# Performance work log

Measured on AMD Instinct MI355X. Metric: run time of the kernel, lower is better.

The kernel has to match this reference:

```python
import jax, jax.numpy as jnp
import numpy as np

N = 50000   # nodes
E = 800000  # edges (avg degree 16)
D = 128     # dim (in == out per layer)
R = 8       # num_relations
B = 4       # num_bases
L = 2       # conv_layer_num
EPS = 1e-5      # LayerNorm eps
SLOPE = 0.2     # leaky_relu negative slope


def setup_inputs() -> dict:
    key = jax.random.key(0)
    ks = jax.random.split(key, 10)
    s = 0.05
    x = jax.random.normal(ks[0], (N, D), dtype=jnp.float32)
    edge_index = jax.random.randint(ks[1], (2, E), 0, N)
    edge_type = jax.random.randint(ks[2], (E,), 0, R)
    basis = jax.random.normal(ks[3], (L, B, D, D), dtype=jnp.float32) * s
    att_r = jax.random.normal(ks[4], (L, R, B), dtype=jnp.float32) * s
    att = jax.random.normal(ks[5], (L, 2 * D), dtype=jnp.float32) * s
    root = jax.random.normal(ks[6], (L, D, D), dtype=jnp.float32) * s
    bias = jax.random.normal(ks[7], (L, D), dtype=jnp.float32) * s
    ln_w = jnp.ones((L, D), dtype=jnp.float32)
    ln_b = jnp.zeros((L, D), dtype=jnp.float32)
    return {"x": x, "edge_index": edge_index, "edge_type": edge_type,
            "basis": basis, "att_r": att_r, "att": att, "root": root,
            "bias": bias, "ln_w": ln_w, "ln_b": ln_b}


def _gnn_layer(x, src, dst, et, basis, att_r, att, root, bias, ln_w, ln_b):
    # relation weights from bases: [R, D, D]
    w = jnp.einsum('rb,bio->rio', att_r, basis)
    # transform all nodes under all relations once, then gather per edge
    xw = jnp.einsum('ni,rio->rno', x, w)          # [R, N, D]
    x_j = xw[et, src]                              # [E, D] relation-specific src msg
    xr = x @ root                                  # [N, D] root transform
    x_i = xr[dst]                                  # [E, D]
    # attention: (cat[x_i, x_j] * att).sum(-1), leaky_relu, segment softmax by dst
    alpha = x_i @ att[:D] + x_j @ att[D:]          # [E]
    alpha = jnp.where(alpha > 0, alpha, SLOPE * alpha)
    amax = jax.ops.segment_max(alpha, dst, num_segments=N)
    amax = jnp.where(jnp.isfinite(amax), amax, 0.0)
    ex = jnp.exp(alpha - amax[dst])
    denom = jax.ops.segment_sum(ex, dst, num_segments=N)
    alpha = ex / (denom[dst] + 1e-16)
    # weighted scatter-add aggregation (dropout rate = 0 -> identity)
    aggr = jax.ops.segment_sum(x_j * alpha[:, None], dst, num_segments=N)  # [N, D]
    out = aggr + xr + bias
    # LayerNorm
    mu = out.mean(-1, keepdims=True)
    var = out.var(-1, keepdims=True)
    out = (out - mu) / jnp.sqrt(var + EPS) * ln_w + ln_b
    return jnp.tanh(out)


def reference(x, edge_index, edge_type, basis, att_r, att, root, bias, ln_w, ln_b):
    src, dst = edge_index[0], edge_index[1]
    states = []
    for l in range(L):
        x = _gnn_layer(x, src, dst, edge_type, basis[l], att_r[l], att[l],
                       root[l], bias[l], ln_w[l], ln_b[l])
        states.append(x)
    return (x, jnp.stack(states))
```

## Files before the change

kernel.cpp:

```cpp
#include <hip/hip_runtime.h>
#include <math.h>

#define D 128
#define NB 4
#define NR 8
#define NLAYER 2
#define KTOT 640
#define EPSV 1e-5f
#define SLOPE 0.2f
#define NBUK 32
#define BSHIFT 11

typedef __attribute__((ext_vector_type(8))) short short8;
typedef __attribute__((ext_vector_type(4))) float f32x4;

__device__ __forceinline__ unsigned short f2bf(float f) {
  unsigned u = __float_as_uint(f);
  u += 0x7FFF + ((u >> 16) & 1);
  return (unsigned short)(u >> 16);
}

__device__ __forceinline__ float block_sum_128(float v, volatile float* scratch) {
#pragma unroll
  for (int off = 32; off > 0; off >>= 1) v += __shfl_xor(v, off);
  __syncthreads();
  if ((threadIdx.x & 63) == 0) scratch[threadIdx.x >> 6] = v;
  __syncthreads();
  return scratch[0] + scratch[1];
}

__global__ void hist_kernel(const int* __restrict__ dst, int* __restrict__ deg, int E) {
  int e = blockIdx.x * 256 + threadIdx.x;
  if (e < E) atomicAdd(&deg[dst[e]], 1);
}

__global__ void __launch_bounds__(1024) scan_kernel(const int* __restrict__ deg,
                                                    int* __restrict__ offs,
                                                    int* __restrict__ cur,
                                                    int* __restrict__ bcur, int n) {
  __shared__ int wsums[16];
  const int tid = threadIdx.x, lane = tid & 63, wid = tid >> 6;
  int carry = 0;
  for (int base = 0; base < n; base += 4096) {
    int i0 = base + tid * 4;
    int v0 = 0, v1 = 0, v2 = 0, v3 = 0;
    if (i0 + 3 < n) {
      int4 q = *(const int4*)(deg + i0);
      v0 = q.x; v1 = q.y; v2 = q.z; v3 = q.w;
    } else if (i0 < n) {
      v0 = deg[i0];
      if (i0 + 1 < n) v1 = deg[i0 + 1];
      if (i0 + 2 < n) v2 = deg[i0 + 2];
    }
    int tsum = v0 + v1 + v2 + v3;
    int x = tsum;
#pragma unroll
    for (int off = 1; off < 64; off <<= 1) {
      int y = __shfl_up(x, off);
      if (lane >= off) x += y;
    }
    if (lane == 63) wsums[wid] = x;
    __syncthreads();
    if (wid == 0) {
      int ws = (lane < 16) ? wsums[lane] : 0;
#pragma unroll
      for (int off = 1; off < 16; off <<= 1) {
        int y = __shfl_up(ws, off);
        if (lane >= off) ws += y;
      }
      if (lane < 16) wsums[lane] = ws;
    }
    __syncthreads();
    int prefix = carry + ((wid > 0) ? wsums[wid - 1] : 0) + x - tsum;
    int e0 = prefix, e1 = e0 + v0, e2 = e1 + v1, e3 = e2 + v2;
    if (i0 < n)     { offs[i0] = e0;     cur[i0] = e0; }
    if (i0 + 1 < n) { offs[i0 + 1] = e1; cur[i0 + 1] = e1; }
    if (i0 + 2 < n) { offs[i0 + 2] = e2; cur[i0 + 2] = e2; }
    if (i0 + 3 < n) { offs[i0 + 3] = e3; cur[i0 + 3] = e3; }
    int btot = wsums[15];
    __syncthreads();
    carry += btot;
  }
  if (tid == 0) offs[n] = carry;
  __syncthreads();
  if (tid < NBUK) {
    int idx = tid << BSHIFT;
    bcur[tid * 16] = offs[idx < n ? idx : n];
  }
}

__global__ void __launch_bounds__(1024) bucket_kernel(
    const int* __restrict__ src, const int* __restrict__ dst, const int* __restrict__ et,
    int* __restrict__ bcur, unsigned long long* __restrict__ ebuf, int E) {
  __shared__ int lcnt[NBUK];
  __shared__ int lbase[NBUK];
  const int tid = threadIdx.x;
  const int e = blockIdx.x * 1024 + tid;
  if (tid < NBUK) lcnt[tid] = 0;
  __syncthreads();
  int d = 0, b = 0, rank = 0;
  unsigned pk = 0;
  bool valid = e < E;
  if (valid) {
    d = dst[e];
    pk = (unsigned)src[e] | ((unsigned)et[e] << 16);
    b = d >> BSHIFT;
    rank = atomicAdd(&lcnt[b], 1);
  }
  __syncthreads();
  if (tid < NBUK && lcnt[tid] > 0) lbase[tid] = atomicAdd(&bcur[tid * 16], lcnt[tid]);
  __syncthreads();
  if (valid) ebuf[lbase[b] + rank] = ((unsigned long long)(unsigned)d << 32) | pk;
}

__global__ void scatter2_kernel(const unsigned long long* __restrict__ ebuf,
                                int* __restrict__ cur, unsigned* __restrict__ csr, int E) {
  int e = blockIdx.x * 256 + threadIdx.x;
  if (e < E) {
    unsigned long long r = ebuf[e];
    int d = (int)(r >> 32);
    int pos = atomicAdd(&cur[d], 1);
    csr[pos] = (unsigned)r;
  }
}

__global__ void __launch_bounds__(128) prep_w(const float* __restrict__ basis,
                                              const float* __restrict__ root,
                                              const float* __restrict__ att,
                                              unsigned short* __restrict__ BT0,
                                              unsigned short* __restrict__ BT1,
                                              float* __restrict__ av0, float* __restrict__ av1) {
  __shared__ float scratch[2];
  int k = blockIdx.x, l = 0;
  if (k >= KTOT) { k -= KTOT; l = 1; }
  const float* basis_l = basis + (size_t)l * NB * D * D;
  const float* root_l  = root + (size_t)l * D * D;
  const float* att_l   = att + (size_t)l * 2 * D;
  unsigned short* BT = l ? BT1 : BT0;
  float* av = l ? av1 : av0;
  const int o = threadIdx.x;
  float v = (k < 512) ? basis_l[(size_t)(k >> 7) * (D * D) + (size_t)(k & 127) * D + o]
                      : root_l[(size_t)(k - 512) * D + o];
  BT[(size_t)o * KTOT + k] = f2bf(v);
  float w = (k < 512) ? att_l[D + o] : att_l[o];
  float s = block_sum_128(v * w, scratch);
  if (o == 0) av[k] = s;
}

__global__ void __launch_bounds__(256) prep_xa(const float* __restrict__ x0,
                                               const float* __restrict__ av,
                                               unsigned short* __restrict__ ga,
                                               float* __restrict__ ai,
                                               float* __restrict__ ajb, int N, int Npad) {
  int n = blockIdx.x * 4 + (threadIdx.x >> 6);
  int lane = threadIdx.x & 63;
  if (n >= Npad) return;
  if (n >= N) {
    *(unsigned*)(ga + (size_t)n * KTOT + 512 + 2 * lane) = 0;
    return;
  }
  float2 xv = *(const float2*)(x0 + (size_t)n * D + 2 * lane);
  unsigned packed = (unsigned)f2bf(xv.x) | ((unsigned)f2bf(xv.y) << 16);
  *(unsigned*)(ga + (size_t)n * KTOT + 512 + 2 * lane) = packed;
  float d[5];
#pragma unroll
  for (int b = 0; b < 4; ++b) {
    float2 w = *(const float2*)(av + b * D + 2 * lane);
    d[b] = xv.x * w.x + xv.y * w.y;
  }
  {
    float2 w = *(const float2*)(av + 512 + 2 * lane);
    d[4] = xv.x * w.x + xv.y * w.y;
  }
#pragma unroll
  for (int off = 1; off < 64; off <<= 1) {
#pragma unroll
    for (int i = 0; i < 5; ++i) d[i] += __shfl_xor(d[i], off);
  }
  if (lane == 0) {
    *(float4*)(ajb + (size_t)n * 4) = make_float4(d[0], d[1], d[2], d[3]);
    ai[n] = d[4];
  }
}

__global__ void __launch_bounds__(256) a2_kernel(const unsigned short* __restrict__ ga,
                                                 const float* __restrict__ av,
                                                 float* __restrict__ ai,
                                                 float* __restrict__ ajb, int N) {
  int n = blockIdx.x * 4 + (threadIdx.x >> 6);
  int lane = threadIdx.x & 63;
  if (n >= N) return;
  unsigned xv = *(const unsigned*)(ga + (size_t)n * KTOT + 512 + 2 * lane);
  float x0 = __uint_as_float(xv << 16);
  float x1 = __uint_as_float(xv & 0xFFFF0000u);
  float d[5];
#pragma unroll
  for (int b = 0; b < 4; ++b) {
    float2 w = *(const float2*)(av + b * D + 2 * lane);
    d[b] = x0 * w.x + x1 * w.y;
  }
  {
    float2 w = *(const float2*)(av + 512 + 2 * lane);
    d[4] = x0 * w.x + x1 * w.y;
  }
#pragma unroll
  for (int off = 1; off < 64; off <<= 1) {
#pragma unroll
    for (int i = 0; i < 5; ++i) d[i] += __shfl_xor(d[i], off);
  }
  if (lane == 0) {
    *(float4*)(ajb + (size_t)n * 4) = make_float4(d[0], d[1], d[2], d[3]);
    ai[n] = d[4];
  }
}

__global__ void __launch_bounds__(256) node_flash(
    unsigned short* __restrict__ ga, const float* __restrict__ ai, const float* __restrict__ ajb,
    const int* __restrict__ offs, const unsigned* __restrict__ csr,
    const float* __restrict__ attr_l, int N) {
  __shared__ float s_c[NR * NB];
  __shared__ float4 s_wc[4][64];
  __shared__ unsigned s_pk[4][64];
  const int w = threadIdx.x >> 6, lane = threadIdx.x & 63;
  const int g = lane >> 4, s = lane & 15;
  const int n = blockIdx.x * 16 + w * 4 + g;
  if (lane < NR * NB) s_c[lane] = attr_l[lane];
  int b0 = 0, b1 = 0;
  float ain = 0.f;
  if (n < N) { b0 = offs[n]; b1 = offs[n + 1]; ain = ai[n]; }
  float ssum = 0.f;
  float acc[4][8];
#pragma unroll
  for (int b = 0; b < 4; ++b)
#pragma unroll
    for (int d = 0; d < 8; ++d) acc[b][d] = 0.f;

  int nch = (b1 - b0 + 15) >> 4;
  nch = max(nch, __shfl_xor(nch, 16));
  nch = max(nch, __shfl_xor(nch, 32));

  for (int ch = 0; ch < nch; ++ch) {
    const int cb = b0 + (ch << 4);
    const int cnt = min(16, b1 - cb);
    float ex = 0.f;
    float4 wc = make_float4(0.f, 0.f, 0.f, 0.f);
    unsigned pk = 0;
    if (s < cnt) {
      pk = csr[cb + s];
      unsigned sn = pk & 0xFFFFu, rt = pk >> 16;
      float4 aj = *(const float4*)(ajb + (size_t)sn * 4);
      float4 cv = *(const float4*)(&s_c[rt * 4]);
      float a = ain + cv.x * aj.x + cv.y * aj.y + cv.z * aj.z + cv.w * aj.w;
      a = fmaxf(a, SLOPE * a);
      ex = __expf(a);
      ssum += ex;
      wc = make_float4(ex * cv.x, ex * cv.y, ex * cv.z, ex * cv.w);
    }
    s_pk[w][lane] = pk;
    s_wc[w][lane] = wc;
    int cc = max(cnt, 0);
    cc = max(cc, __shfl_xor(cc, 16));
    cc = max(cc, __shfl_xor(cc, 32));
    const float4* wrow = &s_wc[w][g * 16];
    const unsigned* prow = &s_pk[w][g * 16];
#pragma unroll 2
    for (int j = 0; j < cc; ++j) {
      float4 wcj = wrow[j];
      unsigned sn = prow[j] & 0xFFFFu;
      const uint4 q = *(const uint4*)(ga + sn * (unsigned)KTOT + 512u + (unsigned)s * 8u);
      float xl, xh;
#define ACC8(K, QQ)                                           \
      xl = __uint_as_float((QQ) << 16);                       \
      xh = __uint_as_float((QQ) & 0xFFFF0000u);               \
      acc[0][2*K]   = fmaf(wcj.x, xl, acc[0][2*K]);           \
      acc[0][2*K+1] = fmaf(wcj.x, xh, acc[0][2*K+1]);         \
      acc[1][2*K]   = fmaf(wcj.y, xl, acc[1][2*K]);           \
      acc[1][2*K+1] = fmaf(wcj.y, xh, acc[1][2*K+1]);         \
      acc[2][2*K]   = fmaf(wcj.z, xl, acc[2][2*K]);           \
      acc[2][2*K+1] = fmaf(wcj.z, xh, acc[2][2*K+1]);         \
      acc[3][2*K]   = fmaf(wcj.w, xl, acc[3][2*K]);           \
      acc[3][2*K+1] = fmaf(wcj.w, xh, acc[3][2*K+1]);
      ACC8(0, q.x) ACC8(1, q.y) ACC8(2, q.z) ACC8(3, q.w)
#undef ACC8
    }
  }
#pragma unroll
  for (int off = 1; off < 16; off <<= 1) ssum += __shfl_xor(ssum, off);
  if (n < N) {
    const float inv = 1.f / (ssum + 1e-16f);
    unsigned short* gp = ga + (size_t)n * KTOT;
#pragma unroll
    for (int b = 0; b < 4; ++b) {
      uint4 r;
      r.x = (unsigned)f2bf(acc[b][0] * inv) | ((unsigned)f2bf(acc[b][1] * inv) << 16);
      r.y = (unsigned)f2bf(acc[b][2] * inv) | ((unsigned)f2bf(acc[b][3] * inv) << 16);
      r.z = (unsigned)f2bf(acc[b][4] * inv) | ((unsigned)f2bf(acc[b][5] * inv) << 16);
      r.w = (unsigned)f2bf(acc[b][6] * inv) | ((unsigned)f2bf(acc[b][7] * inv) << 16);
      *(uint4*)(gp + b * D + s * 8) = r;
    }
  }
}

__global__ void __launch_bounds__(512) gemm2_kernel(
    unsigned short* __restrict__ ga, const unsigned short* __restrict__ BT,
    const float* __restrict__ bias_l, const float* __restrict__ lnw_l,
    const float* __restrict__ lnb_l, float* __restrict__ st,
    float* __restrict__ xfinal, int n_nodes) {
  __shared__ unsigned short sB[128 * 72];
  const int tid = threadIdx.x;
  const int wv = tid >> 6, lane = tid & 63;
  const int l15 = lane & 15, quad = lane >> 4;
  const int rowb = blockIdx.x * 128 + wv * 16;
  const unsigned short* garow = ga + (size_t)(rowb + l15) * KTOT;
  f32x4 acc[8];
  const f32x4 zero = {0.f, 0.f, 0.f, 0.f};
#pragma unroll
  for (int ct = 0; ct < 8; ++ct) acc[ct] = zero;
#pragma unroll
  for (int ch = 0; ch < 10; ++ch) {
    const int k0 = ch * 64;
    short8 a[2];
#pragma unroll
    for (int kc = 0; kc < 2; ++kc)
      a[kc] = *(const short8*)(garow + k0 + kc * 32 + quad * 8);
    __syncthreads();
#pragma unroll
    for (int p = 0; p < 2; ++p) {
      int idx = p * 512 + tid;
      int col = idx >> 3, k8 = idx & 7;
      *(short8*)(sB + col * 72 + k8 * 8) =
          *(const short8*)(BT + (size_t)col * KTOT + k0 + k8 * 8);
    }
    __syncthreads();
#pragma unroll
    for (int kc = 0; kc < 2; ++kc) {
#pragma unroll
      for (int ct = 0; ct < 8; ++ct) {
        const short8* b = (const short8*)(sB + (ct * 16 + l15) * 72 + kc * 32 + quad * 8);
        acc[ct] = __builtin_amdgcn_mfma_f32_16x16x32_bf16(a[kc], *b, acc[ct], 0, 0, 0);
      }
    }
  }
  const int r0 = rowb + quad * 4;
  float bia[8], lw[8], lb[8];
#pragma unroll
  for (int ct = 0; ct < 8; ++ct) {
    int col = ct * 16 + l15;
    bia[ct] = bias_l[col]; lw[ct] = lnw_l[col]; lb[ct] = lnb_l[col];
  }
  float vsum[4] = {0.f, 0.f, 0.f, 0.f}, vsq[4] = {0.f, 0.f, 0.f, 0.f};
#pragma unroll
  for (int ct = 0; ct < 8; ++ct) {
#pragma unroll
    for (int r = 0; r < 4; ++r) {
      float v = acc[ct][r] + bia[ct];
      acc[ct][r] = v;
      vsum[r] += v; vsq[r] += v * v;
    }
  }
#pragma unroll
  for (int r = 0; r < 4; ++r) {
#pragma unroll
    for (int off = 1; off < 16; off <<= 1) {
      vsum[r] += __shfl_xor(vsum[r], off);
      vsq[r]  += __shfl_xor(vsq[r], off);
    }
  }
  float mu[4], rs[4];
#pragma unroll
  for (int r = 0; r < 4; ++r) {
    mu[r] = vsum[r] * (1.0f / D);
    float var = vsq[r] * (1.0f / D) - mu[r] * mu[r];
    rs[r] = rsqrtf(var + EPSV);
  }
#pragma unroll
  for (int ct = 0; ct < 8; ++ct) {
#pragma unroll
    for (int r = 0; r < 4; ++r) {
      int row = r0 + r;
      if (row >= n_nodes) continue;
      int col = ct * 16 + l15;
      float nv = (acc[ct][r] - mu[r]) * rs[r] * lw[ct] + lb[ct];
      float val = tanhf(nv);
      st[(size_t)row * D + col] = val;
      if (xfinal) xfinal[(size_t)row * D + col] = val;
      ga[(size_t)row * KTOT + 512 + col] = f2bf(val);
    }
  }
}

extern "C" void kernel_launch(void* const* d_in, const int* in_sizes, int n_in,
                              void* d_out, int out_size, void* d_ws, size_t ws_size,
                              hipStream_t stream) {
  const float* x0    = (const float*)d_in[0];
  const int*   ei    = (const int*)d_in[1];
  const int*   etype = (const int*)d_in[2];
  const float* basis = (const float*)d_in[3];
  const float* att_r = (const float*)d_in[4];
  const float* att   = (const float*)d_in[5];
  const float* root  = (const float*)d_in[6];
  const float* bias  = (const float*)d_in[7];
  const float* lnw   = (const float*)d_in[8];
  const float* lnb   = (const float*)d_in[9];
  float* out = (float*)d_out;
  const int N = in_sizes[0] / D;
  const int E = in_sizes[2];
  const int Npad = ((N + 127) / 128) * 128;

  char* p = (char*)d_ws;
  auto alloc = [&](size_t bytes) { void* r = (void*)p; p += (bytes + 255) & ~(size_t)255; return r; };
  unsigned short*     ga   = (unsigned short*)alloc((size_t)Npad * KTOT * 2);
  unsigned short*     BT0  = (unsigned short*)alloc((size_t)D * KTOT * 2);
  unsigned short*     BT1  = (unsigned short*)alloc((size_t)D * KTOT * 2);
  float*              av0  = (float*)alloc((size_t)KTOT * 4);
  float*              av1  = (float*)alloc((size_t)KTOT * 4);
  float*              ai   = (float*)alloc((size_t)N * 4);
  float*              ajb  = (float*)alloc((size_t)N * 4 * 4);
  int*                deg  = (int*)alloc((size_t)N * 4);
  int*                offs = (int*)alloc((size_t)(N + 1) * 4);
  int*                cur  = (int*)alloc((size_t)N * 4);
  int*                bcur = (int*)alloc((size_t)NBUK * 16 * 4);
  unsigned*           csr  = (unsigned*)alloc((size_t)E * 4);
  unsigned long long* ebuf = (unsigned long long*)alloc((size_t)E * 8);

  const int* srcp = ei;
  const int* dstp = ei + E;

  hipMemsetAsync(deg, 0, (size_t)N * 4, stream);
  hist_kernel<<<(E + 255) / 256, 256, 0, stream>>>(dstp, deg, E);
  scan_kernel<<<1, 1024, 0, stream>>>(deg, offs, cur, bcur, N);
  bucket_kernel<<<(E + 1023) / 1024, 1024, 0, stream>>>(srcp, dstp, etype, bcur, ebuf, E);
  scatter2_kernel<<<(E + 255) / 256, 256, 0, stream>>>(ebuf, cur, csr, E);

  prep_w<<<2 * KTOT, 128, 0, stream>>>(basis, root, att, BT0, BT1, av0, av1);
  prep_xa<<<Npad / 4, 256, 0, stream>>>(x0, av0, ga, ai, ajb, N, Npad);

  float* states = out + (size_t)N * D;
  for (int l = 0; l < NLAYER; ++l) {
    const unsigned short* BT_l = l ? BT1 : BT0;
    if (l > 0)
      a2_kernel<<<(N + 3) / 4, 256, 0, stream>>>(ga, av1, ai, ajb, N);
    node_flash<<<(N + 15) / 16, 256, 0, stream>>>(ga, ai, ajb, offs, csr,
                                                  att_r + (size_t)l * NR * NB, N);
    float* st = states + (size_t)l * N * D;
    gemm2_kernel<<<Npad / 128, 512, 0, stream>>>(ga, BT_l, bias + (size_t)l * D,
                                                 lnw + (size_t)l * D, lnb + (size_t)l * D,
                                                 st, (l == NLAYER - 1) ? out : nullptr, N);
  }
}
```

Measured before the change: 415.1 us.

## Fuse attention projections into GEMM epilogue and pack FMAs in aggregation

Removes the separate a2_kernel by computing the next layer's attention dot products (ai, ajb) in the gemm2 epilogue from the freshly produced fp32 tanh outputs, avoiding a kernel launch and a re-read of the bf16 node features. node_flash accumulators become float2 vectors so the compiler can emit packed FMA instructions, the inner loop is unrolled further, and the shared-memory rows are padded to 17 entries to reduce bank conflicts. The epilogue gains extra registers and shuffle reductions, and the projections now use fp32 values rather than bf16-rounded ones, which slightly changes numerics.

```diff
diff --git a/kernel.cpp b/kernel.cpp
--- a/kernel.cpp
+++ b/kernel.cpp
@@ -13,6 +13,7 @@
 
 typedef __attribute__((ext_vector_type(8))) short short8;
 typedef __attribute__((ext_vector_type(4))) float f32x4;
+typedef __attribute__((ext_vector_type(2))) float f32x2;
 
 __device__ __forceinline__ unsigned short f2bf(float f) {
   unsigned u = __float_as_uint(f);
@@ -183,66 +184,37 @@
   }
 }
 
-__global__ void __launch_bounds__(256) a2_kernel(const unsigned short* __restrict__ ga,
-                                                 const float* __restrict__ av,
-                                                 float* __restrict__ ai,
-                                                 float* __restrict__ ajb, int N) {
-  int n = blockIdx.x * 4 + (threadIdx.x >> 6);
-  int lane = threadIdx.x & 63;
-  if (n >= N) return;
-  unsigned xv = *(const unsigned*)(ga + (size_t)n * KTOT + 512 + 2 * lane);
-  float x0 = __uint_as_float(xv << 16);
-  float x1 = __uint_as_float(xv & 0xFFFF0000u);
-  float d[5];
-#pragma unroll
-  for (int b = 0; b < 4; ++b) {
-    float2 w = *(const float2*)(av + b * D + 2 * lane);
-    d[b] = x0 * w.x + x1 * w.y;
-  }
-  {
-    float2 w = *(const float2*)(av + 512 + 2 * lane);
-    d[4] = x0 * w.x + x1 * w.y;
-  }
-#pragma unroll
-  for (int off = 1; off < 64; off <<= 1) {
-#pragma unroll
-    for (int i = 0; i < 5; ++i) d[i] += __shfl_xor(d[i], off);
-  }
-  if (lane == 0) {
-    *(float4*)(ajb + (size_t)n * 4) = make_float4(d[0], d[1], d[2], d[3]);
-    ai[n] = d[4];
-  }
-}
-
 __global__ void __launch_bounds__(256) node_flash(
     unsigned short* __restrict__ ga, const float* __restrict__ ai, const float* __restrict__ ajb,
     const int* __restrict__ offs, const unsigned* __restrict__ csr,
     const float* __restrict__ attr_l, int N) {
   __shared__ float s_c[NR * NB];
-  __shared__ float4 s_wc[4][64];
-  __shared__ unsigned s_pk[4][64];
+  __shared__ float4 s_wc[4][68];
+  __shared__ unsigned s_pk[4][68];
   const int w = threadIdx.x >> 6, lane = threadIdx.x & 63;
   const int g = lane >> 4, s = lane & 15;
+  const int gb = g * 17;
   const int n = blockIdx.x * 16 + w * 4 + g;
   if (lane < NR * NB) s_c[lane] = attr_l[lane];
   int b0 = 0, b1 = 0;
   float ain = 0.f;
   if (n < N) { b0 = offs[n]; b1 = offs[n + 1]; ain = ai[n]; }
   float ssum = 0.f;
-  float acc[4][8];
+  f32x2 acc[4][4];
 #pragma unroll
   for (int b = 0; b < 4; ++b)
 #pragma unroll
-    for (int d = 0; d < 8; ++d) acc[b][d] = 0.f;
+    for (int k = 0; k < 4; ++k) acc[b][k] = (f32x2){0.f, 0.f};
 
   int nch = (b1 - b0 + 15) >> 4;
   nch = max(nch, __shfl_xor(nch, 16));
   nch = max(nch, __shfl_xor(nch, 32));
 
+  const unsigned short* gax = ga + 512u + (unsigned)s * 8u;
+
   for (int ch = 0; ch < nch; ++ch) {
     const int cb = b0 + (ch << 4);
     const int cnt = min(16, b1 - cb);
-    float ex = 0.f;
     float4 wc = make_float4(0.f, 0.f, 0.f, 0.f);
     unsigned pk = 0;
     if (s < cnt) {
@@ -252,36 +224,32 @@
       float4 cv = *(const float4*)(&s_c[rt * 4]);
       float a = ain + cv.x * aj.x + cv.y * aj.y + cv.z * aj.z + cv.w * aj.w;
       a = fmaxf(a, SLOPE * a);
-      ex = __expf(a);
+      float ex = __expf(a);
       ssum += ex;
       wc = make_float4(ex * cv.x, ex * cv.y, ex * cv.z, ex * cv.w);
     }
-    s_pk[w][lane] = pk;
-    s_wc[w][lane] = wc;
+    s_pk[w][gb + s] = pk;
+    s_wc[w][gb + s] = wc;
     int cc = max(cnt, 0);
     cc = max(cc, __shfl_xor(cc, 16));
     cc = max(cc, __shfl_xor(cc, 32));
-    const float4* wrow = &s_wc[w][g * 16];
-    const unsigned* prow = &s_pk[w][g * 16];
-#pragma unroll 2
+    const float4* wrow = &s_wc[w][gb];
+    const unsigned* prow = &s_pk[w][gb];
+#pragma unroll 4
     for (int j = 0; j < cc; ++j) {
       float4 wcj = wrow[j];
       unsigned sn = prow[j] & 0xFFFFu;
-      const uint4 q = *(const uint4*)(ga + sn * (unsigned)KTOT + 512u + (unsigned)s * 8u);
-      float xl, xh;
-#define ACC8(K, QQ)                                           \
-      xl = __uint_as_float((QQ) << 16);                       \
-      xh = __uint_as_float((QQ) & 0xFFFF0000u);               \
-      acc[0][2*K]   = fmaf(wcj.x, xl, acc[0][2*K]);           \
-      acc[0][2*K+1] = fmaf(wcj.x, xh, acc[0][2*K+1]);         \
-      acc[1][2*K]   = fmaf(wcj.y, xl, acc[1][2*K]);           \
-      acc[1][2*K+1] = fmaf(wcj.y, xh, acc[1][2*K+1]);         \
-      acc[2][2*K]   = fmaf(wcj.z, xl, acc[2][2*K]);           \
-      acc[2][2*K+1] = fmaf(wcj.z, xh, acc[2][2*K+1]);         \
-      acc[3][2*K]   = fmaf(wcj.w, xl, acc[3][2*K]);           \
-      acc[3][2*K+1] = fmaf(wcj.w, xh, acc[3][2*K+1]);
-      ACC8(0, q.x) ACC8(1, q.y) ACC8(2, q.z) ACC8(3, q.w)
-#undef ACC8
+      const uint4 q = *(const uint4*)(gax + sn * (unsigned)KTOT);
+      f32x2 W0 = {wcj.x, wcj.x}, W1 = {wcj.y, wcj.y};
+      f32x2 W2 = {wcj.z, wcj.z}, W3 = {wcj.w, wcj.w};
+#define ACC2(K, QQ) { \
+      f32x2 X = { __uint_as_float((QQ) << 16), __uint_as_float((QQ) & 0xFFFF0000u) }; \
+      acc[0][K] = __builtin_elementwise_fma(W0, X, acc[0][K]); \
+      acc[1][K] = __builtin_elementwise_fma(W1, X, acc[1][K]); \
+      acc[2][K] = __builtin_elementwise_fma(W2, X, acc[2][K]); \
+      acc[3][K] = __builtin_elementwise_fma(W3, X, acc[3][K]); }
+      ACC2(0, q.x) ACC2(1, q.y) ACC2(2, q.z) ACC2(3, q.w)
+#undef ACC2
     }
   }
 #pragma unroll
@@ -292,10 +260,10 @@
 #pragma unroll
     for (int b = 0; b < 4; ++b) {
       uint4 r;
-      r.x = (unsigned)f2bf(acc[b][0] * inv) | ((unsigned)f2bf(acc[b][1] * inv) << 16);
-      r.y = (unsigned)f2bf(acc[b][2] * inv) | ((unsigned)f2bf(acc[b][3] * inv) << 16);
-      r.z = (unsigned)f2bf(acc[b][4] * inv) | ((unsigned)f2bf(acc[b][5] * inv) << 16);
-      r.w = (unsigned)f2bf(acc[b][6] * inv) | ((unsigned)f2bf(acc[b][7] * inv) << 16);
+      r.x = (unsigned)f2bf(acc[b][0].x * inv) | ((unsigned)f2bf(acc[b][0].y * inv) << 16);
+      r.y = (unsigned)f2bf(acc[b][1].x * inv) | ((unsigned)f2bf(acc[b][1].y * inv) << 16);
+      r.z = (unsigned)f2bf(acc[b][2].x * inv) | ((unsigned)f2bf(acc[b][2].y * inv) << 16);
+      r.w = (unsigned)f2bf(acc[b][3].x * inv) | ((unsigned)f2bf(acc[b][3].y * inv) << 16);
       *(uint4*)(gp + b * D + s * 8) = r;
     }
   }
@@ -305,7 +273,8 @@
     unsigned short* __restrict__ ga, const unsigned short* __restrict__ BT,
     const float* __restrict__ bias_l, const float* __restrict__ lnw_l,
     const float* __restrict__ lnb_l, float* __restrict__ st,
-    float* __restrict__ xfinal, int n_nodes) {
+    float* __restrict__ xfinal, const float* __restrict__ avp,
+    float* __restrict__ ai, float* __restrict__ ajb, int n_nodes) {
   __shared__ unsigned short sB[128 * 72];
   const int tid = threadIdx.x;
   const int wv = tid >> 6, lane = tid & 63;
@@ -373,18 +342,54 @@
     float var = vsq[r] * (1.0f / D) - mu[r] * mu[r];
     rs[r] = rsqrtf(var + EPSV);
   }
+  float part[4][5];
+#pragma unroll
+  for (int r = 0; r < 4; ++r)
+#pragma unroll
+    for (int b = 0; b < 5; ++b) part[r][b] = 0.f;
 #pragma unroll
   for (int ct = 0; ct < 8; ++ct) {
+    int col = ct * 16 + l15;
+    float a0 = 0.f, a1 = 0.f, a2v = 0.f, a3 = 0.f, a4 = 0.f;
+    if (avp) {
+      a0 = avp[col]; a1 = avp[D + col]; a2v = avp[2 * D + col];
+      a3 = avp[3 * D + col]; a4 = avp[4 * D + col];
+    }
 #pragma unroll
     for (int r = 0; r < 4; ++r) {
       int row = r0 + r;
       if (row >= n_nodes) continue;
-      int col = ct * 16 + l15;
       float nv = (acc[ct][r] - mu[r]) * rs[r] * lw[ct] + lb[ct];
       float val = tanhf(nv);
       st[(size_t)row * D + col] = val;
       if (xfinal) xfinal[(size_t)row * D + col] = val;
       ga[(size_t)row * KTOT + 512 + col] = f2bf(val);
+      if (avp) {
+        part[r][0] = fmaf(val, a0, part[r][0]);
+        part[r][1] = fmaf(val, a1, part[r][1]);
+        part[r][2] = fmaf(val, a2v, part[r][2]);
+        part[r][3] = fmaf(val, a3, part[r][3]);
+        part[r][4] = fmaf(val, a4, part[r][4]);
+      }
+    }
+  }
+  if (avp) {
+#pragma unroll
+    for (int off = 1; off < 16; off <<= 1)
+#pragma unroll
+      for (int r = 0; r < 4; ++r)
+#pragma unroll
+        for (int b = 0; b < 5; ++b) part[r][b] += __shfl_xor(part[r][b], off);
+    if (l15 == 0) {
+#pragma unroll
+      for (int r = 0; r < 4; ++r) {
+        int row = r0 + r;
+        if (row < n_nodes) {
+          *(float4*)(ajb + (size_t)row * 4) =
+              make_float4(part[r][0], part[r][1], part[r][2], part[r][3]);
+          ai[row] = part[r][4];
+        }
+      }
     }
   }
 }
@@ -438,13 +443,12 @@
   float* states = out + (size_t)N * D;
   for (int l = 0; l < NLAYER; ++l) {
     const unsigned short* BT_l = l ? BT1 : BT0;
-    if (l > 0)
-      a2_kernel<<<(N + 3) / 4, 256, 0, stream>>>(ga, av1, ai, ajb, N);
     node_flash<<<(N + 15) / 16, 256, 0, stream>>>(ga, ai, ajb, offs, csr,
                                                   att_r + (size_t)l * NR * NB, N);
     float* st = states + (size_t)l * N * D;
     gemm2_kernel<<<Npad / 128, 512, 0, stream>>>(ga, BT_l, bias + (size_t)l * D,
                                                  lnw + (size_t)l * D, lnb + (size_t)l * D,
-                                                 st, (l == NLAYER - 1) ? out : nullptr, N);
-  }
-}
+                                                 st, (l == NLAYER - 1) ? out : nullptr,
+                                                 (l == 0) ? av1 : nullptr, ai, ajb, N);
+  }
+}
```

Measured after the change: 392.8 us. 5.4% less time.
